# Optimization experiments

Measured on AMD Instinct MI355X. Metric: run time of the kernel, lower is better.

Reference implementation:

```python
import jax, jax.numpy as jnp
import numpy as np

EPS = 1e-5

def _conv1x1(x, W, b):
    # x: [B,Ci,H,W], W: [Co,Ci]
    return jnp.einsum('oi,bihw->bohw', W, x) + b[None, :, None, None]

def _bn(x, gamma, beta, mean, var):
    # inference-mode BatchNorm2d
    s = gamma / jnp.sqrt(var + EPS)
    return x * s[None, :, None, None] + (beta - mean * s)[None, :, None, None]

def _conv3x3(x, W, b):
    y = jax.lax.conv_general_dilated(x, W, (1, 1), 'SAME',
                                     dimension_numbers=('NCHW', 'OIHW', 'NCHW'))
    return y + b[None, :, None, None]

def _sparsemax_last(S):
    # sparsemax over the last axis (TrackHSPA: max-subtract, sort, cumsum, threshold)
    S = S - jnp.max(S, axis=-1, keepdims=True)
    srt = -jnp.sort(-S, axis=-1)                 # descending sort
    csum = jnp.cumsum(srt, axis=-1) - 1.0
    N = S.shape[-1]
    ar = jnp.arange(1, N + 1, dtype=S.dtype)
    mask = ar * srt > csum
    k = jnp.sum(mask, axis=-1, keepdims=True)    # support size per row
    tau = jnp.take_along_axis(csum, k - 1, axis=-1) / k.astype(S.dtype)
    return jnp.maximum(S - tau, 0.0)

def _forward(zf, xf, Wq, bq, Ws, bs, Wg, bg, g_gamma, g_beta, g_mean, g_var,
             Wfi, bfi, fi_gamma, fi_beta, fi_mean, fi_var,
             Wm, bm, m_gamma, m_beta, m_mean, m_var, prelu_a):
    B, C, Hx, Wx = xf.shape
    # ---- Graph_Attention_Union (cross-attention) ----
    xf_t = _conv1x1(xf, Wq, bq).reshape(B, C, -1)      # [B,C,Nx]
    zf_t = _conv1x1(zf, Ws, bs).reshape(B, C, -1)      # [B,C,Nz]
    xf_g = jax.nn.relu(_bn(_conv1x1(xf, Wg, bg), g_gamma, g_beta, g_mean, g_var))
    zf_g = jax.nn.relu(_bn(_conv1x1(zf, Wg, bg), g_gamma, g_beta, g_mean, g_var))
    sim = jnp.einsum('bcn,bcm->bnm', xf_t, zf_t)       # [B,Nx,Nz]
    attn = jax.nn.softmax(sim, axis=2)
    emb = jnp.einsum('bcm,bnm->bcn', zf_g.reshape(B, C, -1), attn)
    emb = emb.reshape(B, C, Hx, Wx)
    gat = jax.nn.relu(_bn(_conv1x1(jnp.concatenate([emb, xf_g], axis=1), Wfi, bfi),
                          fi_gamma, fi_beta, fi_mean, fi_var))
    # ---- TrackHSPA (adaptive sparsemax self-attention) ----
    e = _conv3x3(gat, Wm, bm)
    e = _bn(e, m_gamma, m_beta, m_mean, m_var)
    e = jnp.where(e >= 0, e, prelu_a * e)              # PReLU (single param)
    N = Hx * Wx
    ef = e.reshape(B, -1, N)                           # [B,C',N]
    S = jnp.einsum('bdi,bdj->bij', ef, ef)             # [B,N,N]
    P = _sparsemax_last(S)
    out = jnp.einsum('bcn,bnm->bcm', gat.reshape(B, C, N), P)
    return out.reshape(B, C, Hx, Wx) + gat


def setup_inputs():
    key = jax.random.key(0)
    ks = jax.random.split(key, 8)
    B, C, Hz, Wz, Hx, Wx = 32, 256, 7, 7, 31, 31
    Cm = C // 4
    f = lambda k, shape: jax.random.normal(k, shape, jnp.float32) * 0.05
    return {
        'zf': jax.random.normal(ks[0], (B, C, Hz, Wz), jnp.float32),
        'xf': jax.random.normal(ks[1], (B, C, Hx, Wx), jnp.float32),
        'Wq': f(ks[2], (C, C)), 'bq': jnp.zeros((C,), jnp.float32),
        'Ws': f(ks[3], (C, C)), 'bs': jnp.zeros((C,), jnp.float32),
        'Wg': f(ks[4], (C, C)), 'bg': jnp.zeros((C,), jnp.float32),
        'g_gamma': jnp.ones((C,), jnp.float32), 'g_beta': jnp.zeros((C,), jnp.float32),
        'g_mean': jnp.zeros((C,), jnp.float32), 'g_var': jnp.ones((C,), jnp.float32),
        'Wfi': f(ks[5], (C, 2 * C)), 'bfi': jnp.zeros((C,), jnp.float32),
        'fi_gamma': jnp.ones((C,), jnp.float32), 'fi_beta': jnp.zeros((C,), jnp.float32),
        'fi_mean': jnp.zeros((C,), jnp.float32), 'fi_var': jnp.ones((C,), jnp.float32),
        'Wm': f(ks[6], (Cm, C, 3, 3)), 'bm': jnp.zeros((Cm,), jnp.float32),
        'm_gamma': jnp.ones((Cm,), jnp.float32), 'm_beta': jnp.zeros((Cm,), jnp.float32),
        'm_mean': jnp.zeros((Cm,), jnp.float32), 'm_var': jnp.ones((Cm,), jnp.float32),
        'prelu_a': jnp.array(0.25, jnp.float32),
    }


def reference(zf, xf, Wq, bq, Ws, bs, Wg, bg, g_gamma, g_beta, g_mean, g_var,
              Wfi, bfi, fi_gamma, fi_beta, fi_mean, fi_var,
              Wm, bm, m_gamma, m_beta, m_mean, m_var, prelu_a):
    return _forward(zf, xf, Wq, bq, Ws, bs, Wg, bg, g_gamma, g_beta, g_mean, g_var,
                    Wfi, bfi, fi_gamma, fi_beta, fi_mean, fi_var,
                    Wm, bm, m_gamma, m_beta, m_mean, m_var, prelu_a)
```

## Files before the change

### kernel.cpp

```cpp
#include <hip/hip_runtime.h>
#include <cstdint>
#include <cstddef>
#include <math.h>

typedef __attribute__((ext_vector_type(8))) short short8;
typedef __attribute__((ext_vector_type(4))) float floatx4;
typedef unsigned short ushort_t;

__device__ __forceinline__ ushort_t f2bf(float x) {
    union { float f; unsigned u; } v; v.f = x;
    unsigned r = v.u + 0x7FFF + ((v.u >> 16) & 1);
    return (ushort_t)(r >> 16);
}
__device__ __forceinline__ float bf2f(ushort_t h) {
    union { unsigned u; float f; } v; v.u = ((unsigned)h) << 16; return v.f;
}
__device__ __forceinline__ void split2(float v, ushort_t& h, ushort_t& l) {
    h = f2bf(v);
    l = f2bf(v - bf2f(h));
}

#define MFMA(a, b, c) __builtin_amdgcn_mfma_f32_16x16x32_bf16((a), (b), (c), 0, 0, 0)

__device__ __forceinline__ void gload_lds16(const void* g, void* l) {
    __builtin_amdgcn_global_load_lds(
        (const __attribute__((address_space(1))) unsigned*)g,
        (__attribute__((address_space(3))) unsigned*)l, 16, 0, 0);
}

__global__ void prep_all_kernel(
    const float* __restrict__ Wq, const float* __restrict__ Ws,
    const float* __restrict__ Wg, const float* __restrict__ Wfi,
    const float* __restrict__ Wm,
    const float* bq, const float* bs,
    const float* bg, const float* gg, const float* gb, const float* gm, const float* gv,
    const float* bfi, const float* fg, const float* fb, const float* fm, const float* fv,
    const float* bm, const float* mg, const float* mb, const float* mm, const float* mv,
    ushort_t* Wq_h, ushort_t* Wq_l, ushort_t* Ws_h, ushort_t* Ws_l,
    ushort_t* Wg_h, ushort_t* Wg_l, ushort_t* Wfi_h, ushort_t* Wfi_l,
    ushort_t* wm_h, ushort_t* wm_l, float* scsh)
{
    int bid = blockIdx.x, t = threadIdx.x;
    if (bid < 256) {
        int i = bid * 256 + t; ushort_t h, l; split2(Wq[i], h, l); Wq_h[i] = h; Wq_l[i] = l;
    } else if (bid < 512) {
        int i = (bid - 256) * 256 + t; ushort_t h, l; split2(Ws[i], h, l); Ws_h[i] = h; Ws_l[i] = l;
    } else if (bid < 768) {
        int i = (bid - 512) * 256 + t; ushort_t h, l; split2(Wg[i], h, l); Wg_h[i] = h; Wg_l[i] = l;
    } else if (bid < 1280) {
        int i = (bid - 768) * 256 + t; ushort_t h, l; split2(Wfi[i], h, l); Wfi_h[i] = h; Wfi_l[i] = l;
    } else if (bid < 1856) {
        int i = (bid - 1280) * 256 + t;
        int c = i & 255, m = (i >> 8) & 63, tap = i >> 14;
        ushort_t h, l; split2(Wm[((size_t)m * 256 + c) * 9 + tap], h, l);
        wm_h[i] = h; wm_l[i] = l;
    } else {
        if (t < 256) {
            scsh[t] = 1.f;        scsh[256 + t] = bq[t];
            scsh[512 + t] = 1.f;  scsh[768 + t] = bs[t];
            float s = gg[t] * rsqrtf(gv[t] + 1e-5f);
            scsh[1024 + t] = s;   scsh[1280 + t] = gb[t] + s * (bg[t] - gm[t]);
            float s2 = fg[t] * rsqrtf(fv[t] + 1e-5f);
            scsh[1536 + t] = s2;  scsh[1792 + t] = fb[t] + s2 * (bfi[t] - fm[t]);
            if (t < 64) {
                float s3 = mg[t] * rsqrtf(mv[t] + 1e-5f);
                scsh[2048 + t] = s3; scsh[2112 + t] = mb[t] + s3 * (bm[t] - mm[t]);
            }
        }
    }
}

__global__ void halo_zero_kernel(ushort_t* __restrict__ gxh, ushort_t* __restrict__ gxl) {
    int i = blockIdx.x * 256 + threadIdx.x;
    int b = i >> 7, k = i & 127;
    int r;
    if (k < 33) r = k;
    else if (k < 66) r = 32 * 33 + (k - 33);
    else { int k2 = k - 66; r = ((k2 >> 1) + 1) * 33 + ((k2 & 1) ? 32 : 0); }
    uint4* ph = (uint4*)(gxh + ((size_t)b * 1089 + r) * 256);
    uint4* pl = (uint4*)(gxl + ((size_t)b * 1089 + r) * 256);
    uint4 z = make_uint4(0, 0, 0, 0);
#pragma unroll
    for (int s = 0; s < 32; s++) { ph[s] = z; pl[s] = z; }
}

__global__ __launch_bounds__(256) void transpose_in_kernel(
    const float* __restrict__ in, ushort_t* __restrict__ oh, ushort_t* __restrict__ ol,
    int Nsrc, int Npad)
{
    int b = blockIdx.z;
    const float* ib = in + (size_t)b * 256 * Nsrc;
    ushort_t* obh = oh + (size_t)b * Npad * 256;
    ushort_t* obl = ol + (size_t)b * Npad * 256;
    __shared__ float tile[32][33];
    int n0 = blockIdx.x * 32, c0 = blockIdx.y * 32;
    int tx = threadIdx.x & 31, ty = threadIdx.x >> 5;
#pragma unroll
    for (int r = 0; r < 4; r++) {
        int c = c0 + ty + r * 8, n = n0 + tx;
        tile[ty + r * 8][tx] = (n < Nsrc) ? ib[(size_t)c * Nsrc + n] : 0.f;
    }
    __syncthreads();
#pragma unroll
    for (int r = 0; r < 4; r++) {
        int n = n0 + ty + r * 8, c = c0 + tx;
        if (n < Nsrc) {
            ushort_t h, l; split2(tile[tx][ty + r * 8], h, l);
            obh[(size_t)n * 256 + c] = h;
            obl[(size_t)n * 256 + c] = l;
        }
    }
}

__global__ __launch_bounds__(256, 2) void dualconv_mfma_kernel(
    const ushort_t* __restrict__ Xh, const ushort_t* __restrict__ Xl,
    const ushort_t* __restrict__ W1h, const ushort_t* __restrict__ W1l,
    const ushort_t* __restrict__ W2h, const ushort_t* __restrict__ W2l,
    const float* __restrict__ sc1, const float* __restrict__ sh1,
    const float* __restrict__ sc2, const float* __restrict__ sh2,
    int relu1, int relu2,
    ushort_t* __restrict__ O1h, ushort_t* __restrict__ O1l,
    ushort_t* __restrict__ O2h, ushort_t* __restrict__ O2l,
    ushort_t* __restrict__ O2ch, ushort_t* __restrict__ O2cl, int cpitch,
    int K, int Nvalid, int NpadIn, int NpadOut)
{
    __shared__ ushort_t Bs[16384];
    int b = blockIdx.x;
    int n0 = blockIdx.y * 32;
    const ushort_t* Xbh = Xh + (size_t)b * NpadIn * K;
    const ushort_t* Xbl = Xl + (size_t)b * NpadIn * K;
    int tid = threadIdx.x, w = tid >> 6, l = tid & 63, lc = l & 15, q = l >> 4;
    int m0 = w * 64;

#pragma unroll
    for (int r = 0; r < 8; r++) {
        int d = r * 4096 + w * 1024 + l * 16;
        int seg = d >> 14;
        int dr = d & 16383;
        int row = dr >> 9;
        int inrow = (dr & 511) ^ ((row & 7) << 4);
        int srow = n0 + row; if (srow > NpadIn - 1) srow = NpadIn - 1;
        const ushort_t* src = (seg ? Xbl : Xbh) + (size_t)srow * K + (inrow >> 1);
        char* dst = (char*)Bs + (r * 4096 + w * 1024);
        gload_lds16(src, dst);
    }
    __syncthreads();

#define DC_LOADA(K0, AH, AL) do { \
    _Pragma("unroll") \
    for (int mt_ = 0; mt_ < 4; mt_++) { \
        size_t off_ = (size_t)(m0 + mt_ * 16 + lc) * K + (K0) + q * 8; \
        AH[mt_] = *(const short8*)(Wh + off_); \
        AL[mt_] = *(const short8*)(Wl + off_); \
    } \
} while (0)
#define DC_LDSB(K0, BH, BL) do { \
    _Pragma("unroll") \
    for (int jt_ = 0; jt_ < 2; jt_++) { \
        int row_ = jt_ * 16 + lc; \
        int koff_ = (((K0) + q * 8) * 2) ^ ((row_ & 7) << 4); \
        BH[jt_] = *(const short8*)((const char*)Bs + row_ * 512 + koff_); \
        BL[jt_] = *(const short8*)((const char*)Bs + 16384 + row_ * 512 + koff_); \
    } \
} while (0)
#define DC_MFMA(AH, AL, BH, BL) do { \
    _Pragma("unroll") \
    for (int mt_ = 0; mt_ < 4; mt_++) \
    _Pragma("unroll") \
    for (int jt_ = 0; jt_ < 2; jt_++) { \
        acc[mt_][jt_] = MFMA(AH[mt_], BH[jt_], acc[mt_][jt_]); \
        acc[mt_][jt_] = MFMA(AH[mt_], BL[jt_], acc[mt_][jt_]); \
        acc[mt_][jt_] = MFMA(AL[mt_], BH[jt_], acc[mt_][jt_]); \
    } \
} while (0)

    for (int half = 0; half < 2; half++) {
        const ushort_t* Wh = half ? W2h : W1h;
        const ushort_t* Wl = half ? W2l : W1l;
        const float* sc = half ? sc2 : sc1;
        const float* sh = half ? sh2 : sh1;
        int relu = half ? relu2 : relu1;
        ushort_t* Obh = (half ? O2h : O1h) + (size_t)b * NpadOut * 256;
        ushort_t* Obl = (half ? O2l : O1l) + (size_t)b * NpadOut * 256;

        floatx4 acc[4][2];
#pragma unroll
        for (int i = 0; i < 4; i++)
#pragma unroll
            for (int j = 0; j < 2; j++) acc[i][j] = (floatx4){0.f, 0.f, 0.f, 0.f};

        short8 ah0[4], al0[4], ah1[4], al1[4], bh[2], bl[2];
        DC_LOADA(0, ah0, al0);
        for (int k0 = 0; k0 < K; k0 += 64) {
            DC_LOADA(k0 + 32, ah1, al1);
            DC_LDSB(k0, bh, bl);
            DC_MFMA(ah0, al0, bh, bl);
            if (k0 + 64 < K) DC_LOADA(k0 + 64, ah0, al0);
            DC_LDSB(k0 + 32, bh, bl);
            DC_MFMA(ah1, al1, bh, bl);
        }

#pragma unroll
        for (int mt = 0; mt < 4; mt++) {
            int mb = m0 + mt * 16 + q * 4;
            float s0 = sc[mb], s1 = sc[mb + 1], s2 = sc[mb + 2], s3 = sc[mb + 3];
            float h0 = sh[mb], h1 = sh[mb + 1], h2 = sh[mb + 2], h3 = sh[mb + 3];
#pragma unroll
            for (int jt = 0; jt < 2; jt++) {
                int n = n0 + jt * 16 + lc;
                if (n >= Nvalid) continue;
                float v0 = acc[mt][jt][0] * s0 + h0;
                float v1 = acc[mt][jt][1] * s1 + h1;
                float v2 = acc[mt][jt][2] * s2 + h2;
                float v3 = acc[mt][jt][3] * s3 + h3;
                if (relu) { v0 = fmaxf(v0, 0.f); v1 = fmaxf(v1, 0.f); v2 = fmaxf(v2, 0.f); v3 = fmaxf(v3, 0.f); }
                ushort_t e0, f0, e1, f1, e2, f2, e3, f3;
                split2(v0, e0, f0); split2(v1, e1, f1); split2(v2, e2, f2); split2(v3, e3, f3);
                *(ushort4*)(Obh + (size_t)n * 256 + mb) = make_ushort4(e0, e1, e2, e3);
                *(ushort4*)(Obl + (size_t)n * 256 + mb) = make_ushort4(f0, f1, f2, f3);
                if (half && O2ch) {
                    O2ch[((size_t)b * 256 + mb + 0) * cpitch + n] = e0;
                    O2ch[((size_t)b * 256 + mb + 1) * cpitch + n] = e1;
                    O2ch[((size_t)b * 256 + mb + 2) * cpitch + n] = e2;
                    O2ch[((size_t)b * 256 + mb + 3) * cpitch + n] = e3;
                    O2cl[((size_t)b * 256 + mb + 0) * cpitch + n] = f0;
                    O2cl[((size_t)b * 256 + mb + 1) * cpitch + n] = f1;
                    O2cl[((size_t)b * 256 + mb + 2) * cpitch + n] = f2;
                    O2cl[((size_t)b * 256 + mb + 3) * cpitch + n] = f3;
                }
            }
        }
    }
#undef DC_LOADA
#undef DC_LDSB
#undef DC_MFMA
}

__global__ __launch_bounds__(256, 2) void attnfi_mfma_kernel(
    const ushort_t* __restrict__ xth, const ushort_t* __restrict__ xtl,
    const ushort_t* __restrict__ zth, const ushort_t* __restrict__ ztl,
    const ushort_t* __restrict__ zgh, const ushort_t* __restrict__ zgl,
    const ushort_t* __restrict__ Gh, const ushort_t* __restrict__ Gl,
    const ushort_t* __restrict__ Wh, const ushort_t* __restrict__ Wl,
    const float* __restrict__ sc, const float* __restrict__ sh,
    ushort_t* __restrict__ gxh, ushort_t* __restrict__ gxl,
    ushort_t* __restrict__ gat_nf)
{
    __shared__ float SM[32][68];
    __shared__ ushort_t AWh[32][72], AWl[32][72];
    __shared__ ushort_t EM[16384];

    int b = blockIdx.x, nb0 = blockIdx.y * 32;
    int tid = threadIdx.x, w = tid >> 6, l = tid & 63, lc = l & 15, q = l >> 4;
    const ushort_t* xhb = xth + (size_t)b * 992 * 256;
    const ushort_t* xlb = xtl + (size_t)b * 992 * 256;
    const ushort_t* zhb = zth + (size_t)b * 64 * 256;
    const ushort_t* zlb = ztl + (size_t)b * 64 * 256;
    const ushort_t* ghb = zgh + (size_t)b * 256 * 64;
    const ushort_t* glb = zgl + (size_t)b * 256 * 64;
    const ushort_t* Gbh = Gh + (size_t)b * 992 * 256;
    const ushort_t* Gbl = Gl + (size_t)b * 992 * 256;
    ushort_t* gxhb = gxh + (size_t)b * 1089 * 256;
    ushort_t* gxlb = gxl + (size_t)b * 1089 * 256;
    ushort_t* gn = gat_nf + (size_t)b * 256 * 992;
    int m0 = w * 64;

    {
        int rg = w >> 1, c2 = (w & 1) * 2;
        size_t arow = (size_t)(nb0 + rg * 16 + lc) * 256;
        size_t brow0 = (size_t)(c2 * 16 + lc) * 256;
        size_t brow1 = (size_t)((c2 + 1) * 16 + lc) * 256;
        floatx4 s0 = (floatx4){0.f, 0.f, 0.f, 0.f};
        floatx4 s1 = (floatx4){0.f, 0.f, 0.f, 0.f};
        for (int k0 = 0; k0 < 256; k0 += 32) {
            short8 ah = *(const short8*)(xhb + arow + k0 + q * 8);
            short8 al = *(const short8*)(xlb + arow + k0 + q * 8);
            short8 b0h = *(const short8*)(zhb + brow0 + k0 + q * 8);
            short8 b0l = *(const short8*)(zlb + brow0 + k0 + q * 8);
            short8 b1h = *(const short8*)(zhb + brow1 + k0 + q * 8);
            short8 b1l = *(const short8*)(zlb + brow1 + k0 + q * 8);
            s0 = MFMA(ah, b0h, s0); s0 = MFMA(ah, b0l, s0); s0 = MFMA(al, b0h, s0);
            s1 = MFMA(ah, b1h, s1); s1 = MFMA(ah, b1l, s1); s1 = MFMA(al, b1h, s1);
        }
#pragma unroll
        for (int r = 0; r < 4; r++) {
            SM[rg * 16 + q * 4 + r][c2 * 16 + lc] = s0[r];
            SM[rg * 16 + q * 4 + r][(c2 + 1) * 16 + lc] = s1[r];
        }
    }
    __syncthreads();

    if (tid < 32) {
        float mx = -INFINITY;
        for (int m = 0; m < 49; m++) mx = fmaxf(mx, SM[tid][m]);
        float sum = 0.f;
        for (int m = 0; m < 49; m++) { float e = __expf(SM[tid][m] - mx); SM[tid][m] = e; sum += e; }
        float inv = 1.f / sum;
        for (int m = 0; m < 64; m++) {
            float vv = (m < 49) ? SM[tid][m] * inv : 0.f;
            ushort_t hh, ll; split2(vv, hh, ll);
            AWh[tid][m] = hh; AWl[tid][m] = ll;
        }
    }
    __syncthreads();

#pragma unroll
    for (int rg = 0; rg < 2; rg++) {
        short8 pah0 = *(const short8*)(&AWh[rg * 16 + lc][q * 8]);
        short8 pal0 = *(const short8*)(&AWl[rg * 16 + lc][q * 8]);
        short8 pah1 = *(const short8*)(&AWh[rg * 16 + lc][32 + q * 8]);
        short8 pal1 = *(const short8*)(&AWl[rg * 16 + lc][32 + q * 8]);
#pragma unroll
        for (int t = 0; t < 4; t++) {
            int ct = w * 4 + t;
            size_t brow = (size_t)(ct * 16 + lc) * 64;
            short8 bh0 = *(const short8*)(ghb + brow + q * 8);
            short8 bl0 = *(const short8*)(glb + brow + q * 8);
            short8 bh1 = *(const short8*)(ghb + brow + 32 + q * 8);
            short8 bl1 = *(const short8*)(glb + brow + 32 + q * 8);
            floatx4 a = (floatx4){0.f, 0.f, 0.f, 0.f};
            a = MFMA(pah0, bh0, a); a = MFMA(pah0, bl0, a); a = MFMA(pal0, bh0, a);
            a = MFMA(pah1, bh1, a); a = MFMA(pah1, bl1, a); a = MFMA(pal1, bh1, a);
            int cc = ct * 16 + lc;
#pragma unroll
            for (int r = 0; r < 4; r++) {
                int n = rg * 16 + q * 4 + r;
                int off = n * 512 + ((cc * 2) ^ ((n & 7) << 4));
                ushort_t hh, ll; split2(a[r], hh, ll);
                *(ushort_t*)((char*)EM + off) = hh;
                *(ushort_t*)((char*)EM + 16384 + off) = ll;
            }
        }
    }
    __syncthreads();

#define AF_LOADA(K0, AH, AL) do { \
    _Pragma("unroll") \
    for (int mt_ = 0; mt_ < 4; mt_++) { \
        size_t off_ = (size_t)(m0 + mt_ * 16 + lc) * 512 + (K0) + q * 8; \
        AH[mt_] = *(const short8*)(Wh + off_); \
        AL[mt_] = *(const short8*)(Wl + off_); \
    } \
} while (0)
#define AF_LDSB(K0, BH, BL) do { \
    _Pragma("unroll") \
    for (int jt_ = 0; jt_ < 2; jt_++) { \
        int row_ = jt_ * 16 + lc; \
        int koff_ = (((K0) + q * 8) * 2) ^ ((row_ & 7) << 4); \
        BH[jt_] = *(const short8*)((const char*)EM + row_ * 512 + koff_); \
        BL[jt_] = *(const short8*)((const char*)EM + 16384 + row_ * 512 + koff_); \
    } \
} while (0)
#define AF_MFMA(AH, AL, BH, BL) do { \
    _Pragma("unroll") \
    for (int mt_ = 0; mt_ < 4; mt_++) \
    _Pragma("unroll") \
    for (int jt_ = 0; jt_ < 2; jt_++) { \
        acc[mt_][jt_] = MFMA(AH[mt_], BH[jt_], acc[mt_][jt_]); \
        acc[mt_][jt_] = MFMA(AH[mt_], BL[jt_], acc[mt_][jt_]); \
        acc[mt_][jt_] = MFMA(AL[mt_], BH[jt_], acc[mt_][jt_]); \
    } \
} while (0)

    floatx4 acc[4][2];
#pragma unroll
    for (int i = 0; i < 4; i++)
#pragma unroll
        for (int j = 0; j < 2; j++) acc[i][j] = (floatx4){0.f, 0.f, 0.f, 0.f};

    {
        short8 ah0[4], al0[4], ah1[4], al1[4], bh[2], bl[2];
        AF_LOADA(0, ah0, al0);
        for (int kk = 0; kk < 256; kk += 64) {
            AF_LOADA(kk + 32, ah1, al1);
            AF_LDSB(kk, bh, bl);
            AF_MFMA(ah0, al0, bh, bl);
            if (kk + 64 < 256) AF_LOADA(kk + 64, ah0, al0);
            AF_LDSB(kk + 32, bh, bl);
            AF_MFMA(ah1, al1, bh, bl);
        }
    }
    __syncthreads();

#pragma unroll
    for (int r = 0; r < 8; r++) {
        int d = r * 4096 + w * 1024 + l * 16;
        int seg = d >> 14;
        int dr = d & 16383;
        int row = dr >> 9;
        int inrow = (dr & 511) ^ ((row & 7) << 4);
        int srow = nb0 + row; if (srow > 991) srow = 991;
        const ushort_t* src = (seg ? Gbl : Gbh) + (size_t)srow * 256 + (inrow >> 1);
        gload_lds16(src, (char*)EM + d);
    }
    __syncthreads();

    {
        short8 ah0[4], al0[4], ah1[4], al1[4], bh[2], bl[2];
        AF_LOADA(256, ah0, al0);
        for (int kk = 0; kk < 256; kk += 64) {
            AF_LOADA(256 + kk + 32, ah1, al1);
            AF_LDSB(kk, bh, bl);
            AF_MFMA(ah0, al0, bh, bl);
            if (kk + 64 < 256) AF_LOADA(256 + kk + 64, ah0, al0);
            AF_LDSB(kk + 32, bh, bl);
            AF_MFMA(ah1, al1, bh, bl);
        }
    }
#undef AF_LOADA
#undef AF_LDSB
#undef AF_MFMA

#pragma unroll
    for (int mt = 0; mt < 4; mt++) {
        int mb = m0 + mt * 16 + q * 4;
        float s0 = sc[mb], s1 = sc[mb + 1], s2 = sc[mb + 2], s3 = sc[mb + 3];
        float h0 = sh[mb], h1 = sh[mb + 1], h2 = sh[mb + 2], h3 = sh[mb + 3];
#pragma unroll
        for (int jt = 0; jt < 2; jt++) {
            int n = nb0 + jt * 16 + lc;
            if (n >= 961) continue;
            float v0 = fmaxf(acc[mt][jt][0] * s0 + h0, 0.f);
            float v1 = fmaxf(acc[mt][jt][1] * s1 + h1, 0.f);
            float v2 = fmaxf(acc[mt][jt][2] * s2 + h2, 0.f);
            float v3 = fmaxf(acc[mt][jt][3] * s3 + h3, 0.f);
            ushort_t a0, b0, a1, b1, a2, b2, a3, b3;
            split2(v0, a0, b0); split2(v1, a1, b1); split2(v2, a2, b2); split2(v3, a3, b3);
            int hh = n / 31, ww2 = n - hh * 31;
            int row = (hh + 1) * 33 + (ww2 + 1);
            *(ushort4*)(gxhb + (size_t)row * 256 + mb) = make_ushort4(a0, a1, a2, a3);
            *(ushort4*)(gxlb + (size_t)row * 256 + mb) = make_ushort4(b0, b1, b2, b3);
            gn[(size_t)(mb + 0) * 992 + n] = a0;
            gn[(size_t)(mb + 1) * 992 + n] = a1;
            gn[(size_t)(mb + 2) * 992 + n] = a2;
            gn[(size_t)(mb + 3) * 992 + n] = a3;
        }
    }
}

__global__ __launch_bounds__(256, 2) void conv3x3_mfma_kernel(
    const ushort_t* __restrict__ gxh, const ushort_t* __restrict__ gxl,
    const ushort_t* __restrict__ wmh, const ushort_t* __restrict__ wml,
    const float* __restrict__ sc, const float* __restrict__ sh,
    const float* __restrict__ prelu_a,
    ushort_t* __restrict__ eh, ushort_t* __restrict__ el)
{
    __shared__ float Sp[4][2048];
    int b = blockIdx.x;
    const ushort_t* gxhb = gxh + (size_t)b * 1089 * 256;
    const ushort_t* gxlb = gxl + (size_t)b * 1089 * 256;
    ushort_t* ebh = eh + (size_t)b * 1024 * 64;
    ushort_t* ebl = el + (size_t)b * 1024 * 64;
    int tid = threadIdx.x, w = tid >> 6, l = tid & 63, lc = l & 15, q = l >> 4;
    int j0 = blockIdx.y * 64;

    int base[4];
#pragma unroll
    for (int jt = 0; jt < 4; jt++) {
        int j = j0 + jt * 16 + lc; if (j > 960) j = 960;
        int hh = j / 31, ww2 = j - hh * 31;
        base[jt] = (hh + 1) * 33 + (ww2 + 1);
    }

    floatx4 acc[4][4];
#pragma unroll
    for (int i = 0; i < 4; i++)
#pragma unroll
        for (int j = 0; j < 4; j++) acc[i][j] = (floatx4){0.f, 0.f, 0.f, 0.f};

#define C3_LOAD(SL, AH, AL, BH, BL) do { \
    int sl_ = (SL); \
    int tap_ = (sl_ >= 9) ? sl_ - 9 : sl_; \
    int k0_ = (w * 2 + ((sl_ >= 9) ? 1 : 0)) * 32; \
    int doff_ = (tap_ / 3 - 1) * 33 + (tap_ % 3 - 1); \
    const ushort_t* wth_ = wmh + tap_ * 16384; \
    const ushort_t* wtl_ = wml + tap_ * 16384; \
    _Pragma("unroll") \
    for (int mt_ = 0; mt_ < 4; mt_++) { \
        size_t off_ = (size_t)(mt_ * 16 + lc) * 256 + k0_ + q * 8; \
        AH[mt_] = *(const short8*)(wth_ + off_); \
        AL[mt_] = *(const short8*)(wtl_ + off_); \
    } \
    _Pragma("unroll") \
    for (int jt_ = 0; jt_ < 4; jt_++) { \
        size_t off_ = (size_t)(base[jt_] + doff_) * 256 + k0_ + q * 8; \
        BH[jt_] = *(const short8*)(gxhb + off_); \
        BL[jt_] = *(const short8*)(gxlb + off_); \
    } \
} while (0)
#define C3_MFMA(AH, AL, BH, BL) do { \
    _Pragma("unroll") \
    for (int mt_ = 0; mt_ < 4; mt_++) \
    _Pragma("unroll") \
    for (int jt_ = 0; jt_ < 4; jt_++) { \
        acc[mt_][jt_] = MFMA(AH[mt_], BH[jt_], acc[mt_][jt_]); \
        acc[mt_][jt_] = MFMA(AH[mt_], BL[jt_], acc[mt_][jt_]); \
        acc[mt_][jt_] = MFMA(AL[mt_], BH[jt_], acc[mt_][jt_]); \
    } \
} while (0)

    short8 A0h[4], A0l[4], B0h[4], B0l[4];
    short8 A1h[4], A1l[4], B1h[4], B1l[4];
    C3_LOAD(0, A0h, A0l, B0h, B0l);
#pragma unroll
    for (int it = 0; it < 9; it++) {
        C3_LOAD(it * 2 + 1, A1h, A1l, B1h, B1l);
        C3_MFMA(A0h, A0l, B0h, B0l);
        if (it < 8) C3_LOAD(it * 2 + 2, A0h, A0l, B0h, B0l);
        C3_MFMA(A1h, A1l, B1h, B1l);
    }
#undef C3_LOAD
#undef C3_MFMA

    float pa = prelu_a[0];
#pragma unroll
    for (int ph = 0; ph < 2; ph++) {
        __syncthreads();
#pragma unroll
        for (int mt = 0; mt < 4; mt++)
#pragma unroll
            for (int jt = 0; jt < 2; jt++)
#pragma unroll
                for (int r = 0; r < 4; r++)
                    Sp[w][(mt * 16 + q * 4 + r) * 32 + jt * 16 + lc] = acc[mt][ph * 2 + jt][r];
        __syncthreads();
#pragma unroll
        for (int gi = 0; gi < 2; gi++) {
            int g = tid + gi * 256;
            int j = g & 31, mg = g >> 5;
            int m = mg * 4;
            int jj = j0 + ph * 32 + j;
            if (jj >= 961) continue;
            float v[4];
#pragma unroll
            for (int i = 0; i < 4; i++) {
                int idx = (m + i) * 32 + j;
                v[i] = Sp[0][idx] + Sp[1][idx] + Sp[2][idx] + Sp[3][idx];
                v[i] = v[i] * sc[m + i] + sh[m + i];
                v[i] = v[i] >= 0.f ? v[i] : pa * v[i];
            }
            ushort_t a0, b0, a1, b1, a2, b2, a3, b3;
            split2(v[0], a0, b0); split2(v[1], a1, b1);
            split2(v[2], a2, b2); split2(v[3], a3, b3);
            *(ushort4*)(ebh + (size_t)jj * 64 + m) = make_ushort4(a0, a1, a2, a3);
            *(ushort4*)(ebl + (size_t)jj * 64 + m) = make_ushort4(b0, b1, b2, b3);
        }
    }
}

__global__ __launch_bounds__(512) void hspa_mfma_kernel(
    const ushort_t* __restrict__ eh, const ushort_t* __restrict__ el,
    ushort_t* __restrict__ PT)
{
    const int PITCH = 978;
    __shared__ float S[16 * 978];
    int b = blockIdx.x, nb = blockIdx.y;
    const ushort_t* ebh = eh + (size_t)b * 1024 * 64;
    const ushort_t* ebl = el + (size_t)b * 1024 * 64;
    ushort_t* Pb = PT + (size_t)b * 1024 * 992;
    int tid = threadIdx.x, w = tid >> 6, l = tid & 63, lc = l & 15, q = l >> 4;
    int n0 = nb * 32;

    short8 Ah[2][2], Al[2][2];
#pragma unroll
    for (int g = 0; g < 2; g++)
#pragma unroll
        for (int kh = 0; kh < 2; kh++) {
            size_t off = (size_t)(n0 + g * 16 + lc) * 64 + kh * 32 + q * 8;
            Ah[g][kh] = *(const short8*)(ebh + off);
            Al[g][kh] = *(const short8*)(ebl + off);
        }

    floatx4 acc[2][8];
#pragma unroll
    for (int g = 0; g < 2; g++)
#pragma unroll
        for (int s = 0; s < 8; s++) acc[g][s] = (floatx4){0.f, 0.f, 0.f, 0.f};

#define HS_LOADB(SLOT, BH0, BL0, BH1, BL1) do { \
    int jt_ = w + (SLOT) * 8; if (jt_ > 60) jt_ = 60; \
    size_t o_ = (size_t)(jt_ * 16 + lc) * 64 + q * 8; \
    BH0 = *(const short8*)(ebh + o_); \
    BL0 = *(const short8*)(ebl + o_); \
    BH1 = *(const short8*)(ebh + o_ + 32); \
    BL1 = *(const short8*)(ebl + o_ + 32); \
} while (0)

    {
        short8 b0h[2], b0l[2], b1h[2], b1l[2];
        HS_LOADB(0, b0h[0], b0l[0], b1h[0], b1l[0]);
#pragma unroll
        for (int s = 0; s < 8; s++) {
            const int cur = s & 1, nxt = cur ^ 1;
            if (s < 7) HS_LOADB(s + 1, b0h[nxt], b0l[nxt], b1h[nxt], b1l[nxt]);
#pragma unroll
            for (int g = 0; g < 2; g++) {
                floatx4 a = acc[g][s];
                a = MFMA(Ah[g][0], b0h[cur], a);
                a = MFMA(Ah[g][0], b0l[cur], a);
                a = MFMA(Al[g][0], b0h[cur], a);
                a = MFMA(Ah[g][1], b1h[cur], a);
                a = MFMA(Ah[g][1], b1l[cur], a);
                a = MFMA(Al[g][1], b1h[cur], a);
                acc[g][s] = a;
            }
        }
    }
#undef HS_LOADB

#pragma unroll
    for (int g = 0; g < 2; g++) {
        if (g) __syncthreads();
#pragma unroll
        for (int s = 0; s < 8; s++) {
            int jt = w + s * 8;
            if (jt < 61) {
                int j = jt * 16 + lc;
#pragma unroll
                for (int r = 0; r < 4; r++)
                    S[(q * 4 + r) * PITCH + j] = acc[g][s][r];
            }
        }
        __syncthreads();

        int r0 = w * 2, r1 = w * 2 + 1;
        float sv0[16], sv1[16];
        float mx0 = -INFINITY, mx1 = -INFINITY;
#pragma unroll
        for (int t = 0; t < 16; t++) {
            int j = l + t * 64;
            float s0 = (j < 961) ? S[r0 * PITCH + j] : -INFINITY;
            float s1 = (j < 961) ? S[r1 * PITCH + j] : -INFINITY;
            sv0[t] = s0; sv1[t] = s1;
            mx0 = fmaxf(mx0, s0); mx1 = fmaxf(mx1, s1);
        }
        for (int off = 32; off; off >>= 1) {
            mx0 = fmaxf(mx0, __shfl_xor(mx0, off));
            mx1 = fmaxf(mx1, __shfl_xor(mx1, off));
        }
#pragma unroll
        for (int t = 0; t < 16; t++) { sv0[t] -= mx0; sv1[t] -= mx1; }

        float tau0 = -1.f, tau1 = -1.f;
        for (int it = 0; it < 16; it++) {
            float s0 = 0.f, c0 = 0.f, s1 = 0.f, c1 = 0.f;
#pragma unroll
            for (int t = 0; t < 16; t++) {
                if (sv0[t] > tau0) { s0 += sv0[t]; c0 += 1.f; }
                if (sv1[t] > tau1) { s1 += sv1[t]; c1 += 1.f; }
            }
            for (int off = 32; off; off >>= 1) {
                s0 += __shfl_xor(s0, off); c0 += __shfl_xor(c0, off);
                s1 += __shfl_xor(s1, off); c1 += __shfl_xor(c1, off);
            }
            float nt0 = (s0 - 1.f) / c0;
            float nt1 = (s1 - 1.f) / c1;
            bool conv = (nt0 == tau0) && (nt1 == tau1);
            tau0 = nt0; tau1 = nt1;
            if (conv) break;
        }
#pragma unroll
        for (int t = 0; t < 16; t++) {
            int j = l + t * 64;
            if (j < 976) {
                S[r0 * PITCH + j] = (j < 961) ? fmaxf(sv0[t] - tau0, 0.f) : 0.f;
                S[r1 * PITCH + j] = (j < 961) ? fmaxf(sv1[t] - tau1, 0.f) : 0.f;
            }
        }
        __syncthreads();

        int nbase = n0 + g * 16;
        if (nbase < 976) {
            for (int j = tid; j < 976; j += 512) {
                union { ushort_t u[8]; uint4 v; } p0, p1;
#pragma unroll
                for (int r = 0; r < 8; r++)  p0.u[r] = f2bf(S[r * PITCH + j]);
#pragma unroll
                for (int r = 0; r < 8; r++)  p1.u[r] = f2bf(S[(8 + r) * PITCH + j]);
                ushort_t* dst = Pb + (size_t)j * 992 + nbase;
                *(uint4*)(dst) = p0.v;
                *(uint4*)(dst + 8) = p1.v;
            }
        }
    }
}

__global__ __launch_bounds__(256, 2) void out_mfma_kernel(
    const ushort_t* __restrict__ gat_nf, const ushort_t* __restrict__ PT,
    float* __restrict__ out)
{
    int b = blockIdx.x, jb = blockIdx.y;
    const ushort_t* gb = gat_nf + (size_t)b * 256 * 992;
    const ushort_t* Pb = PT + (size_t)b * 1024 * 992;
    float* ob = out + (size_t)b * 256 * 961;
    int tid = threadIdx.x, w = tid >> 6, l = tid & 63, lc = l & 15, q = l >> 4;
    int m0 = w * 64, j0 = jb * 64;

    floatx4 acc[4][4];
#pragma unroll
    for (int i = 0; i < 4; i++)
#pragma unroll
        for (int j = 0; j < 4; j++) acc[i][j] = (floatx4){0.f, 0.f, 0.f, 0.f};

#define OUT_LOAD(K0, AA, BB) do { \
    _Pragma("unroll") \
    for (int mt_ = 0; mt_ < 4; mt_++) \
        AA[mt_] = *(const short8*)(gb + (size_t)(m0 + mt_ * 16 + lc) * 992 + (K0) + q * 8); \
    _Pragma("unroll") \
    for (int jt_ = 0; jt_ < 4; jt_++) \
        BB[jt_] = *(const short8*)(Pb + (size_t)(j0 + jt_ * 16 + lc) * 992 + (K0) + q * 8); \
} while (0)
#define OUT_MFMA(AA, BB) do { \
    _Pragma("unroll") \
    for (int mt_ = 0; mt_ < 4; mt_++) \
    _Pragma("unroll") \
    for (int jt_ = 0; jt_ < 4; jt_++) \
        acc[mt_][jt_] = MFMA(AA[mt_], BB[jt_], acc[mt_][jt_]); \
} while (0)

    short8 a0[4], b0[4], a1[4], b1[4];
    OUT_LOAD(0, a0, b0);
    for (int k0 = 0; k0 < 960; k0 += 64) {
        OUT_LOAD(k0 + 32, a1, b1);
        OUT_MFMA(a0, b0);
        OUT_LOAD(k0 + 64, a0, b0);
        OUT_MFMA(a1, b1);
    }
    OUT_MFMA(a0, b0);
#undef OUT_LOAD
#undef OUT_MFMA

#pragma unroll
    for (int mt = 0; mt < 4; mt++) {
        int mb = m0 + mt * 16 + q * 4;
#pragma unroll
        for (int jt = 0; jt < 4; jt++) {
            int j = j0 + jt * 16 + lc;
            if (j >= 961) continue;
#pragma unroll
            for (int r = 0; r < 4; r++) {
                float g = bf2f(gb[(size_t)(mb + r) * 992 + j]);
                ob[(size_t)(mb + r) * 961 + j] = acc[mt][jt][r] + g;
            }
        }
    }
}

extern "C" void kernel_launch(void* const* d_in, const int* in_sizes, int n_in,
                              void* d_out, int out_size, void* d_ws, size_t ws_size,
                              hipStream_t stream)
{
    const float* zf      = (const float*)d_in[0];
    const float* xf      = (const float*)d_in[1];
    const float* Wq      = (const float*)d_in[2];
    const float* bq      = (const float*)d_in[3];
    const float* Ws      = (const float*)d_in[4];
    const float* bs      = (const float*)d_in[5];
    const float* Wg      = (const float*)d_in[6];
    const float* bg      = (const float*)d_in[7];
    const float* g_gamma = (const float*)d_in[8];
    const float* g_beta  = (const float*)d_in[9];
    const float* g_mean  = (const float*)d_in[10];
    const float* g_var   = (const float*)d_in[11];
    const float* Wfi     = (const float*)d_in[12];
    const float* bfi     = (const float*)d_in[13];
    const float* fi_gamma= (const float*)d_in[14];
    const float* fi_beta = (const float*)d_in[15];
    const float* fi_mean = (const float*)d_in[16];
    const float* fi_var  = (const float*)d_in[17];
    const float* Wm      = (const float*)d_in[18];
    const float* bm      = (const float*)d_in[19];
    const float* m_gamma = (const float*)d_in[20];
    const float* m_beta  = (const float*)d_in[21];
    const float* m_mean  = (const float*)d_in[22];
    const float* m_var   = (const float*)d_in[23];
    const float* prelu_a = (const float*)d_in[24];
    float* out = (float*)d_out;

    ushort_t* ws = (ushort_t*)d_ws;
    ushort_t* Wq_h  = ws + 0;         ushort_t* Wq_l  = ws + 65536;
    ushort_t* Ws_h  = ws + 131072;    ushort_t* Ws_l  = ws + 196608;
    ushort_t* Wg_h  = ws + 262144;    ushort_t* Wg_l  = ws + 327680;
    ushort_t* Wfi_h = ws + 393216;    ushort_t* Wfi_l = ws + 524288;
    ushort_t* wm_h  = ws + 655360;    ushort_t* wm_l  = ws + 802816;
    ushort_t* XT_h    = ws + 950272;
    ushort_t* XT_l    = ws + 9076736;
    ushort_t* xf_tT_h = ws + 17203200;
    ushort_t* xf_tT_l = ws + 25329664;
    ushort_t* zf_tT_h = ws + 33456128;
    ushort_t* zf_tT_l = ws + 33980416;
    ushort_t* zf_gT_h = ws + 34504704;
    ushort_t* zf_gT_l = ws + 35028992;
    ushort_t* xf_gT_h = ws + 35553280;
    ushort_t* xf_gT_l = ws + 43679744;
    ushort_t* gat_nf  = ws + 51806208;
    ushort_t* eT_h    = ws + 59932672;
    ushort_t* eT_l    = ws + 62029824;
    ushort_t* PT      = ws + 64126976;
    ushort_t* gxT_h   = ws + 64126976;
    ushort_t* gxT_l   = ws + 73048064;
    ushort_t* zfT_h   = ws + 96632832;
    ushort_t* zfT_l   = ws + 97157120;
    float* scsh       = (float*)(ws + 97681408);
    ushort_t* zgC_h   = ws + 97685760;
    ushort_t* zgC_l   = ws + 98210048;

    const float* sc_q  = scsh + 0,    *sh_q  = scsh + 256;
    const float* sc_s  = scsh + 512,  *sh_s  = scsh + 768;
    const float* sc_g  = scsh + 1024, *sh_g  = scsh + 1280;
    const float* sc_fi = scsh + 1536, *sh_fi = scsh + 1792;
    const float* sc_m  = scsh + 2048, *sh_m  = scsh + 2112;

    prep_all_kernel<<<1857, 256, 0, stream>>>(
        Wq, Ws, Wg, Wfi, Wm,
        bq, bs, bg, g_gamma, g_beta, g_mean, g_var,
        bfi, fi_gamma, fi_beta, fi_mean, fi_var,
        bm, m_gamma, m_beta, m_mean, m_var,
        Wq_h, Wq_l, Ws_h, Ws_l, Wg_h, Wg_l, Wfi_h, Wfi_l, wm_h, wm_l, scsh);

    transpose_in_kernel<<<dim3(31, 8, 32), 256, 0, stream>>>(xf, XT_h, XT_l, 961, 992);
    transpose_in_kernel<<<dim3(2, 8, 32), 256, 0, stream>>>(zf, zfT_h, zfT_l, 49, 64);

    dualconv_mfma_kernel<<<dim3(32, 31), 256, 0, stream>>>(
        XT_h, XT_l, Wq_h, Wq_l, Wg_h, Wg_l,
        sc_q, sh_q, sc_g, sh_g, 0, 1,
        xf_tT_h, xf_tT_l, xf_gT_h, xf_gT_l,
        nullptr, nullptr, 0, 256, 961, 992, 992);
    dualconv_mfma_kernel<<<dim3(32, 2), 256, 0, stream>>>(
        zfT_h, zfT_l, Ws_h, Ws_l, Wg_h, Wg_l,
        sc_s, sh_s, sc_g, sh_g, 0, 1,
        zf_tT_h, zf_tT_l, zf_gT_h, zf_gT_l,
        zgC_h, zgC_l, 64, 256, 49, 64, 64);

    halo_zero_kernel<<<16, 256, 0, stream>>>(gxT_h, gxT_l);

    attnfi_mfma_kernel<<<dim3(32, 31), 256, 0, stream>>>(
        xf_tT_h, xf_tT_l, zf_tT_h, zf_tT_l, zgC_h, zgC_l,
        xf_gT_h, xf_gT_l, Wfi_h, Wfi_l, sc_fi, sh_fi,
        gxT_h, gxT_l, gat_nf);

    conv3x3_mfma_kernel<<<dim3(32, 16), 256, 0, stream>>>(
        gxT_h, gxT_l, wm_h, wm_l, sc_m, sh_m, prelu_a, eT_h, eT_l);

    hspa_mfma_kernel<<<dim3(32, 31), 512, 0, stream>>>(eT_h, eT_l, PT);

    out_mfma_kernel<<<dim3(32, 16), 256, 0, stream>>>(gat_nf, PT, out);
}
```

Before: 563.4 us.

## Merge xf/zf transpose and dualconv launches; parallelize softmax and shrink attnfi LDS

The xf and zf transposes now run as one kernel launch, and so do the two dual 1x1 conv launches. Each block picks its source, weights and output from its grid index, which removes two launches and lets the small zf work overlap the large xf work. In attnfi, the softmax is split across 64 threads with shuffle reductions instead of 32 serial threads. The bf16 probability rows are packed into the reused SM buffer, which drops the separate AW arrays and lets launch bounds allow 4 blocks per CU. In exchange, the code adds per-block branching and hardcodes the shapes.

Result: faster. 545.2 us (-3.2%).

```diff
diff --git a/kernel.cpp b/kernel.cpp
--- a/kernel.cpp
+++ b/kernel.cpp
@@ -85,15 +85,17 @@
 }
 
 __global__ __launch_bounds__(256) void transpose_in_kernel(
-    const float* __restrict__ in, ushort_t* __restrict__ oh, ushort_t* __restrict__ ol,
-    int Nsrc, int Npad)
+    const float* __restrict__ inA, ushort_t* __restrict__ ohA, ushort_t* __restrict__ olA,
+    const float* __restrict__ inB, ushort_t* __restrict__ ohB, ushort_t* __restrict__ olB)
 {
-    int b = blockIdx.z;
-    const float* ib = in + (size_t)b * 256 * Nsrc;
-    ushort_t* obh = oh + (size_t)b * Npad * 256;
-    ushort_t* obl = ol + (size_t)b * Npad * 256;
+    int bx = blockIdx.x, b = blockIdx.z;
+    int sm = (bx >= 31);
+    int Nsrc = sm ? 49 : 961, Npad = sm ? 64 : 992;
+    const float* ib = (sm ? inB : inA) + (size_t)b * 256 * Nsrc;
+    ushort_t* obh = (sm ? ohB : ohA) + (size_t)b * Npad * 256;
+    ushort_t* obl = (sm ? olB : olA) + (size_t)b * Npad * 256;
     __shared__ float tile[32][33];
-    int n0 = blockIdx.x * 32, c0 = blockIdx.y * 32;
+    int n0 = (sm ? bx - 31 : bx) * 32, c0 = blockIdx.y * 32;
     int tx = threadIdx.x & 31, ty = threadIdx.x >> 5;
 #pragma unroll
     for (int r = 0; r < 4; r++) {
@@ -113,22 +115,28 @@
 }
 
 __global__ __launch_bounds__(256, 2) void dualconv_mfma_kernel(
-    const ushort_t* __restrict__ Xh, const ushort_t* __restrict__ Xl,
-    const ushort_t* __restrict__ W1h, const ushort_t* __restrict__ W1l,
-    const ushort_t* __restrict__ W2h, const ushort_t* __restrict__ W2l,
-    const float* __restrict__ sc1, const float* __restrict__ sh1,
-    const float* __restrict__ sc2, const float* __restrict__ sh2,
-    int relu1, int relu2,
-    ushort_t* __restrict__ O1h, ushort_t* __restrict__ O1l,
-    ushort_t* __restrict__ O2h, ushort_t* __restrict__ O2l,
-    ushort_t* __restrict__ O2ch, ushort_t* __restrict__ O2cl, int cpitch,
-    int K, int Nvalid, int NpadIn, int NpadOut)
+    const ushort_t* __restrict__ XAh, const ushort_t* __restrict__ XAl,
+    const ushort_t* __restrict__ XBh, const ushort_t* __restrict__ XBl,
+    const ushort_t* __restrict__ Wqh, const ushort_t* __restrict__ Wql,
+    const ushort_t* __restrict__ Wsh, const ushort_t* __restrict__ Wsl,
+    const ushort_t* __restrict__ Wgh, const ushort_t* __restrict__ Wgl,
+    const float* __restrict__ scsh,
+    ushort_t* __restrict__ xtA_h, ushort_t* __restrict__ xtA_l,
+    ushort_t* __restrict__ xgA_h, ushort_t* __restrict__ xgA_l,
+    ushort_t* __restrict__ ztB_h, ushort_t* __restrict__ ztB_l,
+    ushort_t* __restrict__ zgB_h, ushort_t* __restrict__ zgB_l,
+    ushort_t* __restrict__ zgC_h, ushort_t* __restrict__ zgC_l)
 {
+    const int K = 256, cpitch = 64;
     __shared__ ushort_t Bs[16384];
     int b = blockIdx.x;
-    int n0 = blockIdx.y * 32;
-    const ushort_t* Xbh = Xh + (size_t)b * NpadIn * K;
-    const ushort_t* Xbl = Xl + (size_t)b * NpadIn * K;
+    int yy = blockIdx.y;
+    int smj = (yy >= 31);
+    int n0 = (smj ? yy - 31 : yy) * 32;
+    int NpadIn = smj ? 64 : 992;
+    int Nvalid = smj ? 49 : 961;
+    const ushort_t* Xbh = (smj ? XBh : XAh) + (size_t)b * NpadIn * K;
+    const ushort_t* Xbl = (smj ? XBl : XAl) + (size_t)b * NpadIn * K;
     int tid = threadIdx.x, w = tid >> 6, l = tid & 63, lc = l & 15, q = l >> 4;
     int m0 = w * 64;
 
@@ -175,13 +183,15 @@
 } while (0)
 
     for (int half = 0; half < 2; half++) {
-        const ushort_t* Wh = half ? W2h : W1h;
-        const ushort_t* Wl = half ? W2l : W1l;
-        const float* sc = half ? sc2 : sc1;
-        const float* sh = half ? sh2 : sh1;
-        int relu = half ? relu2 : relu1;
-        ushort_t* Obh = (half ? O2h : O1h) + (size_t)b * NpadOut * 256;
-        ushort_t* Obl = (half ? O2l : O1l) + (size_t)b * NpadOut * 256;
+        const ushort_t* Wh = half ? Wgh : (smj ? Wsh : Wqh);
+        const ushort_t* Wl = half ? Wgl : (smj ? Wsl : Wql);
+        const float* sc = half ? scsh + 1024 : (smj ? scsh + 512 : scsh + 0);
+        const float* sh = half ? scsh + 1280 : (smj ? scsh + 768 : scsh + 256);
+        int relu = half;
+        ushort_t* Obh = (half ? (smj ? zgB_h : xgA_h) : (smj ? ztB_h : xtA_h))
+                        + (size_t)b * NpadIn * 256;
+        ushort_t* Obl = (half ? (smj ? zgB_l : xgA_l) : (smj ? ztB_l : xtA_l))
+                        + (size_t)b * NpadIn * 256;
 
         floatx4 acc[4][2];
 #pragma unroll
@@ -218,15 +228,15 @@
                 split2(v0, e0, f0); split2(v1, e1, f1); split2(v2, e2, f2); split2(v3, e3, f3);
                 *(ushort4*)(Obh + (size_t)n * 256 + mb) = make_ushort4(e0, e1, e2, e3);
                 *(ushort4*)(Obl + (size_t)n * 256 + mb) = make_ushort4(f0, f1, f2, f3);
-                if (half && O2ch) {
-                    O2ch[((size_t)b * 256 + mb + 0) * cpitch + n] = e0;
-                    O2ch[((size_t)b * 256 + mb + 1) * cpitch + n] = e1;
-                    O2ch[((size_t)b * 256 + mb + 2) * cpitch + n] = e2;
-                    O2ch[((size_t)b * 256 + mb + 3) * cpitch + n] = e3;
-                    O2cl[((size_t)b * 256 + mb + 0) * cpitch + n] = f0;
-                    O2cl[((size_t)b * 256 + mb + 1) * cpitch + n] = f1;
-                    O2cl[((size_t)b * 256 + mb + 2) * cpitch + n] = f2;
-                    O2cl[((size_t)b * 256 + mb + 3) * cpitch + n] = f3;
+                if (half && smj) {
+                    zgC_h[((size_t)b * 256 + mb + 0) * cpitch + n] = e0;
+                    zgC_h[((size_t)b * 256 + mb + 1) * cpitch + n] = e1;
+                    zgC_h[((size_t)b * 256 + mb + 2) * cpitch + n] = e2;
+                    zgC_h[((size_t)b * 256 + mb + 3) * cpitch + n] = e3;
+                    zgC_l[((size_t)b * 256 + mb + 0) * cpitch + n] = f0;
+                    zgC_l[((size_t)b * 256 + mb + 1) * cpitch + n] = f1;
+                    zgC_l[((size_t)b * 256 + mb + 2) * cpitch + n] = f2;
+                    zgC_l[((size_t)b * 256 + mb + 3) * cpitch + n] = f3;
                 }
             }
         }
@@ -236,7 +246,7 @@
 #undef DC_MFMA
 }
 
-__global__ __launch_bounds__(256, 2) void attnfi_mfma_kernel(
+__global__ __launch_bounds__(256, 4) void attnfi_mfma_kernel(
     const ushort_t* __restrict__ xth, const ushort_t* __restrict__ xtl,
     const ushort_t* __restrict__ zth, const ushort_t* __restrict__ ztl,
     const ushort_t* __restrict__ zgh, const ushort_t* __restrict__ zgl,
@@ -246,8 +256,7 @@
     ushort_t* __restrict__ gxh, ushort_t* __restrict__ gxl,
     ushort_t* __restrict__ gat_nf)
 {
-    __shared__ float SM[32][68];
-    __shared__ ushort_t AWh[32][72], AWl[32][72];
+    __shared__ float SM[32][64];
     __shared__ ushort_t EM[16384];
 
     int b = blockIdx.x, nb0 = blockIdx.y * 32;
@@ -290,26 +299,50 @@
     }
     __syncthreads();
 
-    if (tid < 32) {
+    if (tid < 64) {
+        int row = tid & 31, hf = tid >> 5;
+        int mcnt = hf ? 24 : 25;
+        float v[25];
         float mx = -INFINITY;
-        for (int m = 0; m < 49; m++) mx = fmaxf(mx, SM[tid][m]);
+#pragma unroll
+        for (int m = 0; m < 25; m++) {
+            float x = (m < mcnt) ? SM[row][(hf ? 25 : 0) + m] : -INFINITY;
+            v[m] = x; mx = fmaxf(mx, x);
+        }
+        mx = fmaxf(mx, __shfl_xor(mx, 32));
         float sum = 0.f;
-        for (int m = 0; m < 49; m++) { float e = __expf(SM[tid][m] - mx); SM[tid][m] = e; sum += e; }
+#pragma unroll
+        for (int m = 0; m < 25; m++) {
+            float e = (m < mcnt) ? __expf(v[m] - mx) : 0.f;
+            v[m] = e; sum += e;
+        }
+        sum += __shfl_xor(sum, 32);
         float inv = 1.f / sum;
-        for (int m = 0; m < 64; m++) {
-            float vv = (m < 49) ? SM[tid][m] * inv : 0.f;
-            ushort_t hh, ll; split2(vv, hh, ll);
-            AWh[tid][m] = hh; AWl[tid][m] = ll;
+        ushort_t* rowp = (ushort_t*)&SM[row][0];
+        if (hf == 0) {
+#pragma unroll
+            for (int m = 0; m < 25; m++) {
+                ushort_t hh, ll; split2(v[m] * inv, hh, ll);
+                rowp[m] = hh; rowp[64 + m] = ll;
+            }
+        } else {
+#pragma unroll
+            for (int m = 0; m < 39; m++) {
+                float vv = (m < 24) ? v[m] * inv : 0.f;
+                ushort_t hh, ll; split2(vv, hh, ll);
+                rowp[25 + m] = hh; rowp[89 + m] = ll;
+            }
         }
     }
     __syncthreads();
 
 #pragma unroll
     for (int rg = 0; rg < 2; rg++) {
-        short8 pah0 = *(const short8*)(&AWh[rg * 16 + lc][q * 8]);
-        short8 pal0 = *(const short8*)(&AWl[rg * 16 + lc][q * 8]);
-        short8 pah1 = *(const short8*)(&AWh[rg * 16 + lc][32 + q * 8]);
-        short8 pal1 = *(const short8*)(&AWl[rg * 16 + lc][32 + q * 8]);
+        const ushort_t* rowp = (const ushort_t*)&SM[rg * 16 + lc][0];
+        short8 pah0 = *(const short8*)(rowp + q * 8);
+        short8 pal0 = *(const short8*)(rowp + 64 + q * 8);
+        short8 pah1 = *(const short8*)(rowp + 32 + q * 8);
+        short8 pal1 = *(const short8*)(rowp + 96 + q * 8);
 #pragma unroll
         for (int t = 0; t < 4; t++) {
             int ct = w * 4 + t;
@@ -805,9 +838,6 @@
     ushort_t* zgC_h   = ws + 97685760;
     ushort_t* zgC_l   = ws + 98210048;
 
-    const float* sc_q  = scsh + 0,    *sh_q  = scsh + 256;
-    const float* sc_s  = scsh + 512,  *sh_s  = scsh + 768;
-    const float* sc_g  = scsh + 1024, *sh_g  = scsh + 1280;
     const float* sc_fi = scsh + 1536, *sh_fi = scsh + 1792;
     const float* sc_m  = scsh + 2048, *sh_m  = scsh + 2112;
 
@@ -818,19 +848,15 @@
         bm, m_gamma, m_beta, m_mean, m_var,
         Wq_h, Wq_l, Ws_h, Ws_l, Wg_h, Wg_l, Wfi_h, Wfi_l, wm_h, wm_l, scsh);
 
-    transpose_in_kernel<<<dim3(31, 8, 32), 256, 0, stream>>>(xf, XT_h, XT_l, 961, 992);
-    transpose_in_kernel<<<dim3(2, 8, 32), 256, 0, stream>>>(zf, zfT_h, zfT_l, 49, 64);
-
-    dualconv_mfma_kernel<<<dim3(32, 31), 256, 0, stream>>>(
-        XT_h, XT_l, Wq_h, Wq_l, Wg_h, Wg_l,
-        sc_q, sh_q, sc_g, sh_g, 0, 1,
+    transpose_in_kernel<<<dim3(33, 8, 32), 256, 0, stream>>>(
+        xf, XT_h, XT_l, zf, zfT_h, zfT_l);
+
+    dualconv_mfma_kernel<<<dim3(32, 33), 256, 0, stream>>>(
+        XT_h, XT_l, zfT_h, zfT_l,
+        Wq_h, Wq_l, Ws_h, Ws_l, Wg_h, Wg_l, scsh,
         xf_tT_h, xf_tT_l, xf_gT_h, xf_gT_l,
-        nullptr, nullptr, 0, 256, 961, 992, 992);
-    dualconv_mfma_kernel<<<dim3(32, 2), 256, 0, stream>>>(
-        zfT_h, zfT_l, Ws_h, Ws_l, Wg_h, Wg_l,
-        sc_s, sh_s, sc_g, sh_g, 0, 1,
         zf_tT_h, zf_tT_l, zf_gT_h, zf_gT_l,
-        zgC_h, zgC_l, 64, 256, 49, 64, 64);
+        zgC_h, zgC_l);
 
     halo_zero_kernel<<<16, 256, 0, stream>>>(gxT_h, gxT_l);
 
```
